# Performance work log

Hardware: AMD Instinct MI355X
Metric: run time of the kernel (lower is better)

Reference implementation:

```python
import jax, jax.numpy as jnp
import numpy as np

M = 8192          # tokens
DIM = 2048        # per-stream width; K = 4*DIM
S = 4             # fixed stream count (Stream4 kernels)
N = 32            # fixed GEMM output width
SINKHORN_ITERS = 20


def setup_inputs() -> dict:
    key = jax.random.key(0)
    k1, k2 = jax.random.split(key)
    X = jax.random.normal(k1, (M, S * DIM), dtype=jnp.float32)
    # scale W so H = X @ W is O(1): keeps sigmoid/exp/sinkhorn numerically sane
    W = jax.random.normal(k2, (S * DIM, N), dtype=jnp.float32) / np.float32(np.sqrt(S * DIM))
    # module init: beta = zeros(24), alpha = ones(3), concatenated
    alpha_beta = jnp.concatenate([jnp.zeros(24, jnp.float32), jnp.ones(3, jnp.float32)])
    return {"X": X, "W": W, "alpha_beta": alpha_beta}


def _sinkhorn(P, iters=SINKHORN_ITERS):
    # doubly-stochastic normalization of [M, S, S] matrices
    for _ in range(iters):
        P = P / jnp.sum(P, axis=-1, keepdims=True)  # row normalize
        P = P / jnp.sum(P, axis=-2, keepdims=True)  # col normalize
    return P


def reference(X, W, alpha_beta):
    Mm, K = X.shape
    d = K // S
    # skinny GEMM producing the mixing logits (fused w/ SplitK in the kernel)
    H = X @ W                                   # [M, 32]
    b_res, b_pre, b_pos = alpha_beta[0:16], alpha_beta[16:20], alpha_beta[20:24]
    a_res, a_pre, a_pos = alpha_beta[24], alpha_beta[25], alpha_beta[26]
    H_pre = a_pre * jax.nn.sigmoid(H[:, 16:20]) + b_pre          # [M, 4]
    H_pos = a_pos * jax.nn.sigmoid(H[:, 20:24]) + b_pos          # [M, 4]
    H_res = (a_res * H[:, 0:16] + b_res).reshape(Mm, S, S)       # [M, 4, 4]
    H_res = _sinkhorn(jnp.exp(H_res))                            # doubly stochastic
    # view X as 4 streams of width d
    Xs = X.reshape(Mm, S, d)                                     # [M, 4, d]
    # ApplyPreTransform: collapse streams with H_pre weights
    Y = jnp.einsum('ms,msd->md', H_pre, Xs)                      # [M, d]
    # ApplyResidual: per-token 4x4 stream mix + broadcast of pre-transformed feature
    O = jnp.einsum('msi,mid->msd', H_res, Xs) + H_pos[:, :, None] * Y[:, None, :]
    return O.reshape(Mm, K)
```

## Files before the change

### kernel.cpp

```cpp
#include <hip/hip_runtime.h>
#include <math.h>
#include <stdint.h>

#define K_DIM 8192
#define D_DIM 2048
#define M_ROWS 8192
#define N_W 32
#define NC 24
#define KSPLIT 8
#define KRANGE (K_DIM / KSPLIT)
#define KC 256
#define NSTEP (KC / 32)
#define NCHUNK (KRANGE / KC)

typedef short bf16x8 __attribute__((ext_vector_type(8)));
typedef float f32x4 __attribute__((ext_vector_type(4)));

union U32x4 { uint32_t u[4]; bf16x8 v; };

__global__ __launch_bounds__(256) void mhc_gemm_kernel(
    const float* __restrict__ X, const float* __restrict__ W,
    float* __restrict__ Hsum)
{
    __shared__ __align__(16) unsigned short bfr[NSTEP][2][2][64][8];
    const int t = threadIdx.x;
    const int l = t & 63;
    const int wv = t >> 6;
    const int rowbase = blockIdx.x * 64;
    const int kbase = blockIdx.y * KRANGE;

    f32x4 c0 = {0.f, 0.f, 0.f, 0.f};
    f32x4 c1 = {0.f, 0.f, 0.f, 0.f};

    const int arow = rowbase + wv * 16 + (l & 15);
    const float* __restrict__ xrow = X + (size_t)arow * K_DIM + ((l >> 4) * 8);
    const float4* __restrict__ Wg = reinterpret_cast<const float4*>(W);

    for (int c = 0; c < NCHUNK; ++c) {
        __syncthreads();
#pragma unroll
        for (int q = 0; q < 8; ++q) {
            const int f  = q * 256 + t;
            const int kk = f >> 3;
            const int n4 = (f & 7) * 4;
            const float4 wv4 = Wg[(size_t)(kbase + c * KC + kk) * 8 + (f & 7)];
            const float* we = reinterpret_cast<const float*>(&wv4);
            const int s  = kk >> 5;
            const int e  = kk & 7;
            const int lg = (kk >> 3) & 3;
#pragma unroll
            for (int j = 0; j < 4; ++j) {
                const int n = n4 + j;
                const uint32_t u = __float_as_uint(we[j]);
                const float hif = __uint_as_float(u & 0xFFFF0000u);
                const uint32_t ur = __float_as_uint(we[j] - hif);
                bfr[s][n >> 4][0][lg * 16 + (n & 15)][e] = (unsigned short)(u >> 16);
                bfr[s][n >> 4][1][lg * 16 + (n & 15)][e] = (unsigned short)(ur >> 16);
            }
        }
        __syncthreads();

        const float* xc = xrow + kbase + c * KC;
#pragma unroll
        for (int s = 0; s < NSTEP; ++s) {
            const float4 xa = *reinterpret_cast<const float4*>(xc + s * 32);
            const float4 xb = *reinterpret_cast<const float4*>(xc + s * 32 + 4);
            float xs[8];
            xs[0] = xa.x; xs[1] = xa.y; xs[2] = xa.z; xs[3] = xa.w;
            xs[4] = xb.x; xs[5] = xb.y; xs[6] = xb.z; xs[7] = xb.w;

            U32x4 ah, al;
#pragma unroll
            for (int p = 0; p < 4; ++p) {
                const uint32_t u0 = __float_as_uint(xs[2 * p]);
                const uint32_t u1 = __float_as_uint(xs[2 * p + 1]);
                const float h0 = __uint_as_float(u0 & 0xFFFF0000u);
                const float h1 = __uint_as_float(u1 & 0xFFFF0000u);
                const uint32_t r0 = __float_as_uint(xs[2 * p] - h0);
                const uint32_t r1 = __float_as_uint(xs[2 * p + 1] - h1);
                ah.u[p] = (u1 & 0xFFFF0000u) | (u0 >> 16);
                al.u[p] = (r1 & 0xFFFF0000u) | (r0 >> 16);
            }

            const bf16x8 bh0 = *reinterpret_cast<const bf16x8*>(&bfr[s][0][0][l][0]);
            const bf16x8 bl0 = *reinterpret_cast<const bf16x8*>(&bfr[s][0][1][l][0]);
            const bf16x8 bh1 = *reinterpret_cast<const bf16x8*>(&bfr[s][1][0][l][0]);
            const bf16x8 bl1 = *reinterpret_cast<const bf16x8*>(&bfr[s][1][1][l][0]);

            c0 = __builtin_amdgcn_mfma_f32_16x16x32_bf16(ah.v, bh0, c0, 0, 0, 0);
            c0 = __builtin_amdgcn_mfma_f32_16x16x32_bf16(al.v, bh0, c0, 0, 0, 0);
            c0 = __builtin_amdgcn_mfma_f32_16x16x32_bf16(ah.v, bl0, c0, 0, 0, 0);
            c1 = __builtin_amdgcn_mfma_f32_16x16x32_bf16(ah.v, bh1, c1, 0, 0, 0);
            c1 = __builtin_amdgcn_mfma_f32_16x16x32_bf16(al.v, bh1, c1, 0, 0, 0);
            c1 = __builtin_amdgcn_mfma_f32_16x16x32_bf16(ah.v, bl1, c1, 0, 0, 0);
        }
    }

    const int drow = rowbase + wv * 16 + (l >> 4) * 4;
    const int col = l & 15;
#pragma unroll
    for (int r = 0; r < 4; ++r)
        atomicAdd(&Hsum[(size_t)(drow + r) * NC + col], c0[r]);
    if (col < 8) {
#pragma unroll
        for (int r = 0; r < 4; ++r)
            atomicAdd(&Hsum[(size_t)(drow + r) * NC + 16 + col], c1[r]);
    }
}

__global__ __launch_bounds__(256) void mhc_apply_kernel(
    const float* __restrict__ X, const float* __restrict__ Hsum,
    const float* __restrict__ ab, float* __restrict__ out)
{
    __shared__ float pbuf[NC];
    const int row = blockIdx.x;
    const int t = threadIdx.x;

    if (t < 64) {
        const int lane = t;
        const float pl = (lane < NC) ? Hsum[(size_t)row * NC + lane] : 0.f;
        const float bias  = (lane < NC) ? ab[lane] : 0.f;
        const float scale = ab[(lane < 16) ? 24 : ((lane < 20) ? 25 : 26)];

        float vout;
        if (lane < 16) {
            vout = __expf(fmaf(scale, pl, bias));
        } else {
            vout = fmaf(scale, 1.f / (1.f + __expf(-pl)), bias);
        }

        float p = vout;
        for (int it = 0; it < 20; ++it) {
            float rs = p + __shfl_xor(p, 1);
            rs += __shfl_xor(rs, 2);
            p = p / rs;
            float cs = p + __shfl_xor(p, 4);
            cs += __shfl_xor(cs, 8);
            p = p / cs;
        }
        if (lane < NC) pbuf[lane] = (lane < 16) ? p : vout;
    }
    __syncthreads();

    float hres[4][4], hpre[4], hpos[4];
#pragma unroll
    for (int i = 0; i < 16; ++i) hres[i >> 2][i & 3] = pbuf[i];
#pragma unroll
    for (int i = 0; i < 4; ++i) hpre[i] = pbuf[16 + i];
#pragma unroll
    for (int i = 0; i < 4; ++i) hpos[i] = pbuf[20 + i];

    const float4* __restrict__ Xr =
        reinterpret_cast<const float4*>(X + (size_t)row * K_DIM);
    float4* __restrict__ Or = reinterpret_cast<float4*>(out + (size_t)row * K_DIM);

#pragma unroll
    for (int q = 0; q < 2; ++q) {
        const int pos = t + q * 256;
        float4 xq[4];
#pragma unroll
        for (int i = 0; i < 4; ++i) xq[i] = Xr[i * (D_DIM / 4) + pos];

        float y[4];
#pragma unroll
        for (int e = 0; e < 4; ++e) {
            float s = 0.f;
#pragma unroll
            for (int i = 0; i < 4; ++i)
                s = fmaf(hpre[i], reinterpret_cast<const float*>(&xq[i])[e], s);
            y[e] = s;
        }

#pragma unroll
        for (int s = 0; s < 4; ++s) {
            float4 o;
            float* oe = reinterpret_cast<float*>(&o);
#pragma unroll
            for (int e = 0; e < 4; ++e) {
                float v = hpos[s] * y[e];
#pragma unroll
                for (int i = 0; i < 4; ++i)
                    v = fmaf(hres[s][i], reinterpret_cast<const float*>(&xq[i])[e], v);
                oe[e] = v;
            }
            Or[s * (D_DIM / 4) + pos] = o;
        }
    }
}

extern "C" void kernel_launch(void* const* d_in, const int* in_sizes, int n_in,
                              void* d_out, int out_size, void* d_ws, size_t ws_size,
                              hipStream_t stream) {
    const float* X  = (const float*)d_in[0];
    const float* W  = (const float*)d_in[1];
    const float* ab = (const float*)d_in[2];
    float* out = (float*)d_out;
    float* Hsum = (float*)d_ws;

    hipMemsetAsync(d_ws, 0, (size_t)M_ROWS * NC * sizeof(float), stream);
    dim3 g1(M_ROWS / 64, KSPLIT);
    mhc_gemm_kernel<<<g1, 256, 0, stream>>>(X, W, Hsum);
    mhc_apply_kernel<<<M_ROWS, 256, 0, stream>>>(X, Hsum, ab, out);
}
```

Before: 179.4 us.

## Prepack W into bf16 hi/lo MFMA fragments once and drop per-block LDS staging

A new prepack kernel splits W into bf16 high/low parts laid out in MFMA B-fragment order in workspace, and also zeroes Hsum, which replaces the memset call. The GEMM kernel then loads the B fragments straight from global memory (they should stay in cache) instead of every block converting W into shared memory behind two barriers per chunk. This removes redundant W conversion across all 128 row blocks and the __syncthreads stalls. The cost is one extra launch and per-lane global loads of B in the inner loop, which lean on L2/L1 hits.

```diff
diff --git a/kernel.cpp b/kernel.cpp
--- a/kernel.cpp
+++ b/kernel.cpp
@@ -9,91 +9,88 @@
 #define NC 24
 #define KSPLIT 8
 #define KRANGE (K_DIM / KSPLIT)
-#define KC 256
-#define NSTEP (KC / 32)
-#define NCHUNK (KRANGE / KC)
+#define NKSTEP (KRANGE / 32)
+#define TOTAL_KSTEPS (K_DIM / 32)
 
 typedef short bf16x8 __attribute__((ext_vector_type(8)));
 typedef float f32x4 __attribute__((ext_vector_type(4)));
-
 union U32x4 { uint32_t u[4]; bf16x8 v; };
 
-__global__ __launch_bounds__(256) void mhc_gemm_kernel(
-    const float* __restrict__ X, const float* __restrict__ W,
+#define WFRAG_IDX(ks, tile, hilo) ((((ks) * 2 + (tile)) * 2 + (hilo)) * 64)
+
+__global__ __launch_bounds__(256) void mhc_prepack_kernel(
+    const float* __restrict__ W, unsigned short* __restrict__ wfrag,
     float* __restrict__ Hsum)
 {
-    __shared__ __align__(16) unsigned short bfr[NSTEP][2][2][64][8];
+    const int idx = blockIdx.x * 256 + threadIdx.x;
+    const int k = idx >> 5, n = idx & 31;
+    const float w = W[(size_t)k * N_W + n];
+    const uint32_t u = __float_as_uint(w);
+    const float hif = __uint_as_float(u & 0xFFFF0000u);
+    const uint32_t ur = __float_as_uint(w - hif);
+
+    const int ks = k >> 5, kk = k & 31;
+    const int lane = ((kk >> 3) << 4) | (n & 15);
+    const int e = kk & 7;
+    const int tile = n >> 4;
+    unsigned short* p = wfrag + ((size_t)WFRAG_IDX(ks, tile, 0) + lane) * 8 + e;
+    p[0]   = (unsigned short)(u >> 16);
+    p[512] = (unsigned short)(ur >> 16);
+
+    if (idx < M_ROWS * NC) Hsum[idx] = 0.f;
+}
+
+__global__ __launch_bounds__(256) void mhc_gemm_kernel(
+    const float* __restrict__ X, const unsigned short* __restrict__ wfrag,
+    float* __restrict__ Hsum)
+{
     const int t = threadIdx.x;
     const int l = t & 63;
     const int wv = t >> 6;
     const int rowbase = blockIdx.x * 64;
-    const int kbase = blockIdx.y * KRANGE;
+    const int ks0 = blockIdx.y * NKSTEP;
 
     f32x4 c0 = {0.f, 0.f, 0.f, 0.f};
     f32x4 c1 = {0.f, 0.f, 0.f, 0.f};
 
     const int arow = rowbase + wv * 16 + (l & 15);
     const float* __restrict__ xrow = X + (size_t)arow * K_DIM + ((l >> 4) * 8);
-    const float4* __restrict__ Wg = reinterpret_cast<const float4*>(W);
-
-    for (int c = 0; c < NCHUNK; ++c) {
-        __syncthreads();
-#pragma unroll
-        for (int q = 0; q < 8; ++q) {
-            const int f  = q * 256 + t;
-            const int kk = f >> 3;
-            const int n4 = (f & 7) * 4;
-            const float4 wv4 = Wg[(size_t)(kbase + c * KC + kk) * 8 + (f & 7)];
-            const float* we = reinterpret_cast<const float*>(&wv4);
-            const int s  = kk >> 5;
-            const int e  = kk & 7;
-            const int lg = (kk >> 3) & 3;
-#pragma unroll
-            for (int j = 0; j < 4; ++j) {
-                const int n = n4 + j;
-                const uint32_t u = __float_as_uint(we[j]);
-                const float hif = __uint_as_float(u & 0xFFFF0000u);
-                const uint32_t ur = __float_as_uint(we[j] - hif);
-                bfr[s][n >> 4][0][lg * 16 + (n & 15)][e] = (unsigned short)(u >> 16);
-                bfr[s][n >> 4][1][lg * 16 + (n & 15)][e] = (unsigned short)(ur >> 16);
-            }
-        }
-        __syncthreads();
-
-        const float* xc = xrow + kbase + c * KC;
-#pragma unroll
-        for (int s = 0; s < NSTEP; ++s) {
-            const float4 xa = *reinterpret_cast<const float4*>(xc + s * 32);
-            const float4 xb = *reinterpret_cast<const float4*>(xc + s * 32 + 4);
-            float xs[8];
-            xs[0] = xa.x; xs[1] = xa.y; xs[2] = xa.z; xs[3] = xa.w;
-            xs[4] = xb.x; xs[5] = xb.y; xs[6] = xb.z; xs[7] = xb.w;
-
-            U32x4 ah, al;
-#pragma unroll
-            for (int p = 0; p < 4; ++p) {
-                const uint32_t u0 = __float_as_uint(xs[2 * p]);
-                const uint32_t u1 = __float_as_uint(xs[2 * p + 1]);
-                const float h0 = __uint_as_float(u0 & 0xFFFF0000u);
-                const float h1 = __uint_as_float(u1 & 0xFFFF0000u);
-                const uint32_t r0 = __float_as_uint(xs[2 * p] - h0);
-                const uint32_t r1 = __float_as_uint(xs[2 * p + 1] - h1);
-                ah.u[p] = (u1 & 0xFFFF0000u) | (u0 >> 16);
-                al.u[p] = (r1 & 0xFFFF0000u) | (r0 >> 16);
-            }
-
-            const bf16x8 bh0 = *reinterpret_cast<const bf16x8*>(&bfr[s][0][0][l][0]);
-            const bf16x8 bl0 = *reinterpret_cast<const bf16x8*>(&bfr[s][0][1][l][0]);
-            const bf16x8 bh1 = *reinterpret_cast<const bf16x8*>(&bfr[s][1][0][l][0]);
-            const bf16x8 bl1 = *reinterpret_cast<const bf16x8*>(&bfr[s][1][1][l][0]);
-
-            c0 = __builtin_amdgcn_mfma_f32_16x16x32_bf16(ah.v, bh0, c0, 0, 0, 0);
-            c0 = __builtin_amdgcn_mfma_f32_16x16x32_bf16(al.v, bh0, c0, 0, 0, 0);
-            c0 = __builtin_amdgcn_mfma_f32_16x16x32_bf16(ah.v, bl0, c0, 0, 0, 0);
-            c1 = __builtin_amdgcn_mfma_f32_16x16x32_bf16(ah.v, bh1, c1, 0, 0, 0);
-            c1 = __builtin_amdgcn_mfma_f32_16x16x32_bf16(al.v, bh1, c1, 0, 0, 0);
-            c1 = __builtin_amdgcn_mfma_f32_16x16x32_bf16(ah.v, bl1, c1, 0, 0, 0);
-        }
+    const bf16x8* __restrict__ wf = reinterpret_cast<const bf16x8*>(wfrag);
+
+#pragma unroll 2
+    for (int s = 0; s < NKSTEP; ++s) {
+        const int ks = ks0 + s;
+        const float* xc = xrow + ks * 32;
+        const float4 xa = *reinterpret_cast<const float4*>(xc);
+        const float4 xb = *reinterpret_cast<const float4*>(xc + 4);
+        float xs[8];
+        xs[0] = xa.x; xs[1] = xa.y; xs[2] = xa.z; xs[3] = xa.w;
+        xs[4] = xb.x; xs[5] = xb.y; xs[6] = xb.z; xs[7] = xb.w;
+
+        U32x4 ah, al;
+#pragma unroll
+        for (int p = 0; p < 4; ++p) {
+            const uint32_t u0 = __float_as_uint(xs[2 * p]);
+            const uint32_t u1 = __float_as_uint(xs[2 * p + 1]);
+            const float h0 = __uint_as_float(u0 & 0xFFFF0000u);
+            const float h1 = __uint_as_float(u1 & 0xFFFF0000u);
+            const uint32_t r0 = __float_as_uint(xs[2 * p] - h0);
+            const uint32_t r1 = __float_as_uint(xs[2 * p + 1] - h1);
+            ah.u[p] = (u1 & 0xFFFF0000u) | (u0 >> 16);
+            al.u[p] = (r1 & 0xFFFF0000u) | (r0 >> 16);
+        }
+
+        const bf16x8 bh0 = wf[WFRAG_IDX(ks, 0, 0) + l];
+        const bf16x8 bl0 = wf[WFRAG_IDX(ks, 0, 1) + l];
+        const bf16x8 bh1 = wf[WFRAG_IDX(ks, 1, 0) + l];
+        const bf16x8 bl1 = wf[WFRAG_IDX(ks, 1, 1) + l];
+
+        c0 = __builtin_amdgcn_mfma_f32_16x16x32_bf16(ah.v, bh0, c0, 0, 0, 0);
+        c0 = __builtin_amdgcn_mfma_f32_16x16x32_bf16(al.v, bh0, c0, 0, 0, 0);
+        c0 = __builtin_amdgcn_mfma_f32_16x16x32_bf16(ah.v, bl0, c0, 0, 0, 0);
+        c1 = __builtin_amdgcn_mfma_f32_16x16x32_bf16(ah.v, bh1, c1, 0, 0, 0);
+        c1 = __builtin_amdgcn_mfma_f32_16x16x32_bf16(al.v, bh1, c1, 0, 0, 0);
+        c1 = __builtin_amdgcn_mfma_f32_16x16x32_bf16(ah.v, bl1, c1, 0, 0, 0);
     }
 
     const int drow = rowbase + wv * 16 + (l >> 4) * 4;
@@ -196,9 +193,10 @@
     const float* ab = (const float*)d_in[2];
     float* out = (float*)d_out;
     float* Hsum = (float*)d_ws;
-
-    hipMemsetAsync(d_ws, 0, (size_t)M_ROWS * NC * sizeof(float), stream);
+    unsigned short* wfrag = (unsigned short*)((char*)d_ws + (size_t)M_ROWS * NC * 4);
+
+    mhc_prepack_kernel<<<(K_DIM * N_W) / 256, 256, 0, stream>>>(W, wfrag, Hsum);
     dim3 g1(M_ROWS / 64, KSPLIT);
-    mhc_gemm_kernel<<<g1, 256, 0, stream>>>(X, W, Hsum);
+    mhc_gemm_kernel<<<g1, 256, 0, stream>>>(X, wfrag, Hsum);
     mhc_apply_kernel<<<M_ROWS, 256, 0, stream>>>(X, Hsum, ab, out);
 }
```

After: 183.4 us. +2.2%, slower.
